# Performance work log

Measured on AMD Instinct MI355X. Metric: run time of the kernel, lower is better.

## Reference

```python
import math
import jax, jax.numpy as jnp
import numpy as np

NH, D, MULT, VOCAB, NLAYER = 4, 256, 128, 256, 2
N = MULT * D // NH  # 8192
EPS = 1e-5
THETA = 2.0 ** 16


def get_freqs(n):
    q = (jnp.arange(n, dtype=jnp.float32) // 2) * 2  # quantize(t, 2)
    return 1.0 / (THETA ** (q / n)) / (2 * math.pi)


def ln(x):
    # LayerNorm over last dim, no affine
    mu = jnp.mean(x, axis=-1, keepdims=True)
    var = jnp.mean((x - mu) ** 2, axis=-1, keepdims=True)
    return (x - mu) / jnp.sqrt(var + EPS)


def rope(phases, v):
    # phases: (T, N), v: (B, nh, T, N)
    ph = (phases % 1.0) * (2 * math.pi)
    c, s = jnp.cos(ph), jnp.sin(ph)
    v_rot = jnp.stack((-v[..., 1::2], v[..., ::2]), axis=-1).reshape(v.shape)
    return v * c + v_rot * s


def setup_inputs() -> dict:
    key = jax.random.key(0)
    ks = jax.random.split(key, 6)
    std = 0.02
    return {
        "idx": jax.random.randint(ks[0], (1, 2048), 0, VOCAB),
        "embed": jax.random.normal(ks[1], (VOCAB, D), jnp.float32) * std,
        "encoder": jax.random.normal(ks[2], (NH, D, N), jnp.float32) * std,
        "encoder_v": jax.random.normal(ks[3], (NH, D, N), jnp.float32) * std,
        "decoder": jax.random.normal(ks[4], (NH * N, D), jnp.float32) * std,
        "lm_head": jax.random.normal(ks[5], (D, VOCAB), jnp.float32) * std,
    }


def reference(idx, embed, encoder, encoder_v, decoder, lm_head):
    B, T = idx.shape
    freqs = get_freqs(N)  # (N,)
    phases = jnp.arange(T, dtype=jnp.float32)[:, None] * freqs[None, :]  # (T, N)
    # strictly-lower-triangular causal mask (tril diagonal=-1)
    t = jnp.arange(T)
    mask = (t[:, None] > t[None, :]).astype(jnp.float32)  # (T, T)

    x = ln(embed[idx][:, None])  # (B, 1, T, D)
    for _ in range(NLAYER):
        x_sparse = jax.nn.relu(jnp.einsum('bltd,hdn->bhtn', x, encoder))  # (B,nh,T,N)
        QR = rope(phases, x_sparse)
        scores = jnp.einsum('bhtn,bhsn->bhts', QR, QR) * mask  # (B,nh,T,T)
        yKV = ln(jnp.einsum('bhts,blsd->bhtd', scores, x))  # (B,nh,T,D)
        y_sparse = jax.nn.relu(jnp.einsum('bhtd,hdn->bhtn', yKV, encoder_v))
        xy = x_sparse * y_sparse  # (B,nh,T,N)
        xy = xy.transpose(0, 2, 1, 3).reshape(B, 1, T, NH * N)
        yMLP = xy @ decoder  # (B,1,T,D)
        x = ln(x + ln(yMLP))
    logits = x[:, 0] @ lm_head  # (B,T,vocab)
    return logits
```

## Files before the change

### kernel.cpp

```cpp
#include <hip/hip_runtime.h>
#include <hip/hip_bf16.h>
#include <math.h>

typedef unsigned short u16;
typedef unsigned int u32;
typedef __attribute__((ext_vector_type(8))) short short8;
typedef __attribute__((ext_vector_type(4))) float f32x4;
typedef __attribute__((ext_vector_type(4))) unsigned short u16x4;

__device__ __forceinline__ u16 f2b(float f) {
  u32 u = __builtin_bit_cast(u32, f);
  u = (u + 0x7fffu + ((u >> 16) & 1u)) >> 16;
  return (u16)u;
}
__device__ __forceinline__ float b2f(u16 s) {
  return __builtin_bit_cast(float, (u32)s << 16);
}

__device__ __forceinline__ void ld_g2l(const u16* g, u16* l) {
  __builtin_amdgcn_global_load_lds(
      (const __attribute__((address_space(1))) unsigned int*)g,
      (__attribute__((address_space(3))) unsigned int*)l, 16, 0, 0);
}

__device__ __forceinline__ float rope_frev(int n) {
  return exp2f((float)(-(n & ~1)) * (1.0f / 512.0f)) * 0.15915494f;
}
__device__ __forceinline__ void rope_cs_fast(float frev, int t, float& c, float& s) {
  float ph = (float)t * frev;
  ph -= floorf(ph);
#if __has_builtin(__builtin_amdgcn_sinf) && __has_builtin(__builtin_amdgcn_cosf)
  s = __builtin_amdgcn_sinf(ph);
  c = __builtin_amdgcn_cosf(ph);
#else
  __sincosf(ph * 6.2831853f, &s, &c);
#endif
}

__device__ __forceinline__ void gemm_core(
    const u16* __restrict__ A, const u16* __restrict__ B,
    int lda, int ldb, int Klen, int kb, int bm, int bn,
    u16* __restrict__ As, u16* __restrict__ Bs, f32x4 (&acc)[4][4])
{
  int tid = threadIdx.x;
  int w = tid >> 6, lane = tid & 63;
  int srow = (w << 4) + (lane >> 2);
  int scol = (lane & 3) << 3;
  const u16* ga0 = A + (long)(bm * 128 + srow) * lda + kb + scol;
  const u16* ga1 = ga0 + (long)64 * lda;
  const u16* gb0 = B + (long)(bn * 128 + srow) * ldb + kb + scol;
  const u16* gb1 = gb0 + (long)64 * ldb;
  u16* la0 = As + (w << 9);  u16* la1 = la0 + 2048;
  u16* lb0 = Bs + (w << 9);  u16* lb1 = lb0 + 2048;

  int wm = (w >> 1) << 6, wn = (w & 1) << 6;
  int lane15 = lane & 15, quad = lane >> 4;
  const u16* ar = As + (wm + lane15) * 32 + quad * 8;
  const u16* br = Bs + (wn + lane15) * 32 + quad * 8;

#pragma unroll
  for (int i = 0; i < 4; i++)
#pragma unroll
    for (int j = 0; j < 4; j++) { f32x4 z = {0.f, 0.f, 0.f, 0.f}; acc[i][j] = z; }

  for (int k = 0; k < Klen; k += 64) {
    ld_g2l(ga0 + k, la0);
    ld_g2l(ga1 + k, la1);
    ld_g2l(gb0 + k, lb0);
    ld_g2l(gb1 + k, lb1);
    ld_g2l(ga0 + k + 32, la0 + 4096);
    ld_g2l(ga1 + k + 32, la1 + 4096);
    ld_g2l(gb0 + k + 32, lb0 + 4096);
    ld_g2l(gb1 + k + 32, lb1 + 4096);
    __syncthreads();
#pragma unroll
    for (int h = 0; h < 2; h++) {
      short8 af[4], bfr[4];
#pragma unroll
      for (int mt = 0; mt < 4; mt++) af[mt] = *(const short8*)(ar + h * 4096 + mt * 16 * 32);
#pragma unroll
      for (int nt = 0; nt < 4; nt++) bfr[nt] = *(const short8*)(br + h * 4096 + nt * 16 * 32);
#pragma unroll
      for (int mt = 0; mt < 4; mt++)
#pragma unroll
        for (int nt = 0; nt < 4; nt++)
          acc[mt][nt] = __builtin_amdgcn_mfma_f32_16x16x32_bf16(af[mt], bfr[nt], acc[mt][nt], 0, 0, 0);
    }
    __syncthreads();
  }
}

template<int EPI>
__global__ __launch_bounds__(256, 2) void gemm_bt(
    const u16* __restrict__ A, const u16* __restrict__ B, void* __restrict__ C,
    int K, int lda, int ldb, int ldc, int nsplits, long aB, long bB, long cB,
    int tri)
{
  __shared__ __align__(16) u16 As[2 * 128 * 32];
  __shared__ __align__(16) u16 Bs[2 * 128 * 32];
  int bn = blockIdx.x, bm = blockIdx.y;
  int batch = blockIdx.z / nsplits, sp = blockIdx.z % nsplits;
  int Klen = K / nsplits, kb = sp * Klen;
  if (tri) {
    int kend = (bm + 1) * 128;
    if (kb >= kend) return;
    if (kb + Klen > kend) Klen = kend - kb;
  }

  f32x4 acc[4][4];
  gemm_core(A + (long)batch * aB, B + (long)batch * bB, lda, ldb, Klen, kb, bm, bn, As, Bs, acc);

  int lane = threadIdx.x & 63, w = threadIdx.x >> 6;
  int wm = (w >> 1) << 6, wn = (w & 1) << 6;
  int lane15 = lane & 15, quad = lane >> 4;

  float frev[4] = {0.f, 0.f, 0.f, 0.f};
  if (EPI == 1 || EPI == 4) {
#pragma unroll
    for (int nt = 0; nt < 4; nt++)
      frev[nt] = rope_frev(bn * 128 + wn + nt * 16 + lane15);
  }

#pragma unroll
  for (int mt = 0; mt < 4; mt++)
#pragma unroll
    for (int nt = 0; nt < 4; nt++) {
      int gn = bn * 128 + wn + nt * 16 + lane15;
#pragma unroll
      for (int r = 0; r < 4; r++) {
        int gm = bm * 128 + wm + mt * 16 + quad * 4 + r;
        float v = acc[mt][nt][r];
        long ci = (long)batch * cB + (long)gm * ldc + gn;
        if (EPI == 0) {
          ((float*)C)[ci] = v;
        } else if (EPI == 1) {
          float rv = fmaxf(v, 0.f);
          float ro = __shfl_xor(rv, 1);
          float c, s; rope_cs_fast(frev[nt], gm, c, s);
          float out = (gn & 1) ? (rv * c + ro * s) : (rv * c - ro * s);
          ((u16*)C)[ci] = f2b(out);
        } else if (EPI == 3) {
          atomicAdd(&((float*)C)[ci], v);
        } else if (EPI == 4) {
          u16* Cp = (u16*)C;
          float q = b2f(Cp[ci]);
          float qo = __shfl_xor(q, 1);
          float c, s; rope_cs_fast(frev[nt], gm, c, s);
          float xs = (gn & 1) ? (q * c - qo * s) : (q * c + qo * s);
          Cp[ci] = f2b(fmaxf(v, 0.f) * xs);
        }
      }
    }
}

#define SC_BAR   __builtin_amdgcn_s_barrier()
#define SC_LGKM0 asm volatile("s_waitcnt lgkmcnt(0)" ::: "memory")
#define SC_LGKM8 asm volatile("s_waitcnt lgkmcnt(8)" ::: "memory")
#define SC_VMF   do { asm volatile("s_waitcnt vmcnt(4)" ::: "memory"); \
                      __builtin_amdgcn_sched_barrier(0); } while (0)
#define SC_P1    __builtin_amdgcn_s_setprio(1)
#define SC_P0    __builtin_amdgcn_s_setprio(0)

#define DSA(Ab, mh) { \
  _Pragma("unroll") for (int mt = 0; mt < 4; mt++) { \
    aA[mt][0] = *(const short8*)((Ab) + ((mh) * 64 + mt * 16) * 64 + koff0); \
    aA[mt][1] = *(const short8*)((Ab) + ((mh) * 64 + mt * 16) * 64 + koff1); } }

#define DSB(Bb, nh, dst) { \
  _Pragma("unroll") for (int nt = 0; nt < 2; nt++) { \
    dst[nt][0] = *(const short8*)((Bb) + ((nh) * 32 + nt * 16) * 64 + koff0); \
    dst[nt][1] = *(const short8*)((Bb) + ((nh) * 32 + nt * 16) * 64 + koff1); } }

#define MMA(MH, NH, BB) { \
  _Pragma("unroll") for (int mt = 0; mt < 4; mt++) \
  _Pragma("unroll") for (int nt = 0; nt < 2; nt++) { \
    acc[(MH)*4+mt][(NH)*2+nt] = __builtin_amdgcn_mfma_f32_16x16x32_bf16( \
        aA[mt][0], BB[nt][0], acc[(MH)*4+mt][(NH)*2+nt], 0, 0, 0); \
    acc[(MH)*4+mt][(NH)*2+nt] = __builtin_amdgcn_mfma_f32_16x16x32_bf16( \
        aA[mt][1], BB[nt][1], acc[(MH)*4+mt][(NH)*2+nt], 0, 0, 0); } }

#define SCORES_K_LOOP(kb, nkt) \
  for (int i = 0; i < (nkt) / 2; i++) { \
    int kt1 = (kb) + 2 * i + 1; \
    int kt2 = 2 * i + 2; if (kt2 > (nkt) - 1) kt2 = (nkt) - 1; kt2 += (kb); \
    int kt3 = 2 * i + 3; if (kt3 > (nkt) - 1) kt3 = (nkt) - 1; kt3 += (kb); \
    short8 aA[4][2], bb0[2][2], bb1[2][2]; \
     \
    DSA(A0, 0); DSB(B0, 0, bb0); \
    STG(gA, &Abuf[1][0], kt1); \
    SC_LGKM8; SC_BAR; SC_LGKM0; SC_P1; MMA(0, 0, bb0); SC_P0; SC_BAR; \
     \
    DSB(B0, 1, bb1); \
    STG(gA + HSTEP, &Abuf[1][128 * 64], kt1); \
    SC_BAR; SC_LGKM0; SC_P1; MMA(0, 1, bb1); SC_P0; SC_BAR; \
     \
    DSA(A0, 1); \
    STG(gB, &Bbuf[0][0], kt2); \
    SC_BAR; SC_LGKM0; SC_P1; MMA(1, 1, bb1); SC_P0; SC_BAR; \
     \
    STG(gB + HSTEP, &Bbuf[0][128 * 64], kt2); \
    SC_VMF; SC_BAR; SC_LGKM0; SC_P1; MMA(1, 0, bb0); SC_P0; SC_BAR; \
     \
    DSA(A1, 0); DSB(B1, 0, bb0); \
    STG(gA, &Abuf[0][0], kt2); \
    SC_LGKM8; SC_BAR; SC_LGKM0; SC_P1; MMA(0, 0, bb0); SC_P0; SC_BAR; \
     \
    DSB(B1, 1, bb1); \
    STG(gA + HSTEP, &Abuf[0][128 * 64], kt2); \
    SC_BAR; SC_LGKM0; SC_P1; MMA(0, 1, bb1); SC_P0; SC_BAR; \
     \
    DSA(A1, 1); \
    STG(gB, &Bbuf[1][0], kt3); \
    SC_BAR; SC_LGKM0; SC_P1; MMA(1, 1, bb1); SC_P0; SC_BAR; \
     \
    STG(gB + HSTEP, &Bbuf[1][128 * 64], kt3); \
    SC_VMF; SC_BAR; SC_LGKM0; SC_P1; MMA(1, 0, bb0); SC_P0; SC_BAR; \
  }

#define SCORES_SETUP \
  int tid = threadIdx.x; \
  int w = tid >> 6, lane = tid & 63; \
  int wr = w >> 2, wc = w & 3; \
  int lane15 = lane & 15, quad = lane >> 4; \
  int swz = lane15 & 7; \
  int koff0 = ((quad) ^ swz) << 3; \
  int koff1 = ((4 + quad) ^ swz) << 3; \
  const u16* gA = Q + (long)(bm * 256) * 8192; \
  const u16* gB = Q + (long)(bn * 256) * 8192; \
  const u16* A0 = &Abuf[0][(wr * 128 + lane15) * 64]; \
  const u16* A1 = &Abuf[1][(wr * 128 + lane15) * 64]; \
  const u16* B0 = &Bbuf[0][(wc * 64 + lane15) * 64]; \
  const u16* B1 = &Bbuf[1][(wc * 64 + lane15) * 64]; \
  int sr = lane >> 3, sc = lane & 7; \
  long g_sk = (long)sr * 8192 + ((sc ^ sr) << 3); \
  int l_base = (w * 16) * 64; \
  long g_wrow = (long)(w * 16) * 8192; \
  auto STG = [&](const u16* gHalfBase, u16* lHalfBase, int kt) { \
    const u16* g = gHalfBase + g_wrow + g_sk + (long)kt * 64; \
    u16* l = lHalfBase + l_base; \
    ld_g2l(g, l); \
    ld_g2l(g + (long)8 * 8192, l + 8 * 64); \
  }; \
  f32x4 acc[8][4]; \
  _Pragma("unroll") \
  for (int i2 = 0; i2 < 8; i2++) \
  _Pragma("unroll") \
    for (int j = 0; j < 4; j++) { f32x4 z = {0.f, 0.f, 0.f, 0.f}; acc[i2][j] = z; } \
  const long HSTEP = (long)128 * 8192;

__device__ __forceinline__ void tri_decode(int q, int& bm, int& bn) {
  bm = (int)((sqrtf(8.f * (float)q + 1.f) - 1.f) * 0.5f);
  while ((bm + 1) * (bm + 2) / 2 <= q) bm++;
  while (bm * (bm + 1) / 2 > q) bm--;
  bn = q - bm * (bm + 1) / 2;
}

__device__ __forceinline__ int xcd_remap(int lin, int total) {
  int cpx = total >> 3, rr = total & 7;
  int xcd = lin & 7, ii = lin >> 3;
  return (xcd < rr) ? xcd * (cpx + 1) + ii
                    : rr * (cpx + 1) + (xcd - rr) * cpx + ii;
}

__global__ __launch_bounds__(512, 1) void gemm_scores8(
    const u16* __restrict__ QR, u16* __restrict__ S, int T, int ntri)
{
  __shared__ __align__(16) u16 Abuf[2][256 * 64];
  __shared__ __align__(16) u16 Bbuf[2][256 * 64];

  int c = xcd_remap(blockIdx.x, gridDim.x);
  int zh = c / ntri, q = c % ntri;
  int bm, bn; tri_decode(q, bm, bn);

  const u16* Q = QR + (long)zh * (long)T * 8192;
  u16* Sb = S + (long)zh * (long)T * T;

  SCORES_SETUP

  STG(gA, &Abuf[0][0], 0); STG(gA + HSTEP, &Abuf[0][128 * 64], 0);
  STG(gB, &Bbuf[0][0], 0); STG(gB + HSTEP, &Bbuf[0][128 * 64], 0);
  STG(gB, &Bbuf[1][0], 1); STG(gB + HSTEP, &Bbuf[1][128 * 64], 1);
  SC_VMF;
  SC_BAR;

  SCORES_K_LOOP(0, 128)

#pragma unroll
  for (int mt = 0; mt < 8; mt++)
#pragma unroll
    for (int nt = 0; nt < 4; nt++) {
      int gn = bn * 256 + wc * 64 + nt * 16 + lane15;
#pragma unroll
      for (int r = 0; r < 4; r++) {
        int gm = bm * 256 + wr * 128 + mt * 16 + quad * 4 + r;
        Sb[(long)gm * T + gn] = f2b(gm > gn ? acc[mt][nt][r] : 0.f);
      }
    }
}

__global__ __launch_bounds__(512, 1) void gemm_scores_k3(
    const u16* __restrict__ QR, float* __restrict__ Sf, int T, int ntri)
{
  __shared__ __align__(16) u16 Abuf[2][256 * 64];
  __shared__ __align__(16) u16 Bbuf[2][256 * 64];

  int c = xcd_remap(blockIdx.x, gridDim.x);
  int sp = c % 3, c2 = c / 3;
  int zh = c2 / ntri, q = c2 % ntri;
  int bm, bn; tri_decode(q, bm, bn);

  int kb = sp * 44;
  int nkt = (sp == 2) ? 40 : 44;

  const u16* Q = QR + (long)zh * (long)T * 8192;
  float* Sb = Sf + (long)zh * (long)T * T;

  SCORES_SETUP

  STG(gA, &Abuf[0][0], kb); STG(gA + HSTEP, &Abuf[0][128 * 64], kb);
  STG(gB, &Bbuf[0][0], kb); STG(gB + HSTEP, &Bbuf[0][128 * 64], kb);
  STG(gB, &Bbuf[1][0], kb + 1); STG(gB + HSTEP, &Bbuf[1][128 * 64], kb + 1);
  SC_VMF;
  SC_BAR;

  SCORES_K_LOOP(kb, nkt)

#pragma unroll
  for (int mt = 0; mt < 8; mt++)
#pragma unroll
    for (int nt = 0; nt < 4; nt++) {
      int gn = bn * 256 + wc * 64 + nt * 16 + lane15;
#pragma unroll
      for (int r = 0; r < 4; r++) {
        int gm = bm * 256 + wr * 128 + mt * 16 + quad * 4 + r;
        atomicAdd(&Sb[(long)gm * T + gn], acc[mt][nt][r]);
      }
    }
}

__global__ __launch_bounds__(256) void tril_cvt(
    const float* __restrict__ Sf, u16* __restrict__ Sb, int T, int ntri)
{
  int bx = blockIdx.x;
  int tl = bx >> 3, chunk = bx & 7;
  int zh = tl / ntri, q = tl % ntri;
  int bm, bn; tri_decode(q, bm, bn);
  const float* f = Sf + (long)zh * (long)T * T;
  u16* b = Sb + (long)zh * (long)T * T;
  int tid = threadIdx.x;
  int rsub = tid >> 6;
  int col = bn * 256 + (tid & 63) * 4;
#pragma unroll
  for (int it = 0; it < 8; it++) {
    int row = bm * 256 + chunk * 32 + it * 4 + rsub;
    long o = (long)row * T + col;
    f32x4 v = *(const f32x4*)(f + o);
    u16x4 w2;
#pragma unroll
    for (int r = 0; r < 4; r++)
      w2[r] = (row > col + r) ? f2b(v[r]) : (u16)0;
    *(u16x4*)(b + o) = w2;
  }
}

__global__ __launch_bounds__(256) void trans_f32_bf16(
    const float* __restrict__ src, u16* __restrict__ dst, int R, int C)
{
  __shared__ float tile[32][33];
  long off = (long)blockIdx.z * R * C;
  const float* s = src + off;
  u16* d = dst + off;
  int lx = threadIdx.x & 31, ly = threadIdx.x >> 5;
  int c = blockIdx.x * 32 + lx;
#pragma unroll
  for (int p = 0; p < 32; p += 8)
    tile[ly + p][lx] = s[(long)(blockIdx.y * 32 + ly + p) * C + c];
  __syncthreads();
  int rr = blockIdx.y * 32 + lx;
#pragma unroll
  for (int p = 0; p < 32; p += 8)
    d[(long)(blockIdx.x * 32 + ly + p) * R + rr] = f2b(tile[lx][ly + p]);
}

__device__ __forceinline__ float block_sum(float v, float* red) {
#pragma unroll
  for (int o = 32; o > 0; o >>= 1) v += __shfl_down(v, o, 64);
  int lane = threadIdx.x & 63, wid = threadIdx.x >> 6;
  if (lane == 0) red[wid] = v;
  __syncthreads();
  float r = red[0] + red[1] + red[2] + red[3];
  __syncthreads();
  return r;
}

__global__ __launch_bounds__(256) void embed_ln(
    const int* __restrict__ idx, const float* __restrict__ embed,
    float* __restrict__ x, u16* __restrict__ xb, u16* __restrict__ xT, int T)
{
  __shared__ float red[4];
  int t = blockIdx.x, d = threadIdx.x;
  float v = embed[(long)idx[t] * 256 + d];
  float mu = block_sum(v, red) * (1.f / 256.f);
  float c = v - mu;
  float var = block_sum(c * c, red) * (1.f / 256.f);
  float o = c * rsqrtf(var + 1e-5f);
  x[(long)t * 256 + d] = o;
  xb[(long)t * 256 + d] = f2b(o);
  xT[(long)d * T + t] = f2b(o);
}

__global__ __launch_bounds__(256) void row_ln(
    const float* __restrict__ in, u16* __restrict__ out)
{
  __shared__ float red[4];
  long row = blockIdx.x;
  int d = threadIdx.x;
  float v = in[row * 256 + d];
  float mu = block_sum(v, red) * (1.f / 256.f);
  float c = v - mu;
  float var = block_sum(c * c, red) * (1.f / 256.f);
  out[row * 256 + d] = f2b(c * rsqrtf(var + 1e-5f));
}

__global__ __launch_bounds__(256) void resid_ln(
    const float* __restrict__ yMLP, float* __restrict__ x,
    u16* __restrict__ xb, u16* __restrict__ xT, int T)
{
  __shared__ float red[4];
  int t = blockIdx.x, d = threadIdx.x;
  float y = yMLP[(long)t * 256 + d];
  float mu1 = block_sum(y, red) * (1.f / 256.f);
  float c1 = y - mu1;
  float var1 = block_sum(c1 * c1, red) * (1.f / 256.f);
  float l1 = c1 * rsqrtf(var1 + 1e-5f);
  float v = x[(long)t * 256 + d] + l1;
  float mu2 = block_sum(v, red) * (1.f / 256.f);
  float c2 = v - mu2;
  float var2 = block_sum(c2 * c2, red) * (1.f / 256.f);
  float o = c2 * rsqrtf(var2 + 1e-5f);
  x[(long)t * 256 + d] = o;
  xb[(long)t * 256 + d] = f2b(o);
  xT[(long)d * T + t] = f2b(o);
}

extern "C" void kernel_launch(void* const* d_in, const int* in_sizes, int n_in,
                              void* d_out, int out_size, void* d_ws, size_t ws_size,
                              hipStream_t stream) {
  const int*   idx       = (const int*)d_in[0];
  const float* embed     = (const float*)d_in[1];
  const float* encoder   = (const float*)d_in[2];
  const float* encoder_v = (const float*)d_in[3];
  const float* decoder   = (const float*)d_in[4];
  const float* lm_head   = (const float*)d_in[5];
  const int T = in_sizes[0];
  const int D = 256, NH = 4, Nn = 8192, V = 256;

  char* ws = (char*)d_ws;
  size_t off = 0;
  auto alloc = [&](size_t bytes) -> void* {
    void* p = ws + off; off += (bytes + 255) & ~(size_t)255; return p;
  };
  float* x_f32   = (float*)alloc((size_t)T * D * 4);
  float* yMLP    = (float*)alloc((size_t)T * D * 4);
  float* yKV_f32 = (float*)alloc((size_t)NH * T * D * 4);
  u16* x_b    = (u16*)alloc((size_t)T * D * 2);
  u16* xT     = (u16*)alloc((size_t)T * D * 2);
  u16* yKV_b  = (u16*)alloc((size_t)NH * T * D * 2);
  u16* lmT    = (u16*)alloc((size_t)D * V * 2);
  u16* encT   = (u16*)alloc((size_t)NH * Nn * D * 2);
  u16* encvT  = (u16*)alloc((size_t)NH * Nn * D * 2);
  u16* decT   = (u16*)alloc((size_t)D * NH * Nn * 2);
  size_t per_head = ((size_t)T * T * 2 + 256) + ((size_t)T * Nn * 2 + 256);
  int HB = 4;
  while (HB > 1 && off + (size_t)HB * per_head > ws_size) HB >>= 1;
  u16* scores = (u16*)alloc((size_t)HB * T * T * 2);
  u16* QRxy   = (u16*)alloc((size_t)HB * T * Nn * 2);
  if (off > ws_size) return;
  float* scoresF = nullptr;
  {
    size_t need = (size_t)HB * T * T * 4 + 256;
    if (off + need <= ws_size) scoresF = (float*)alloc((size_t)HB * T * T * 4);
  }

  trans_f32_bf16<<<dim3(Nn / 32, D / 32, NH), 256, 0, stream>>>(encoder, encT, D, Nn);
  trans_f32_bf16<<<dim3(Nn / 32, D / 32, NH), 256, 0, stream>>>(encoder_v, encvT, D, Nn);
  trans_f32_bf16<<<dim3(D / 32, (NH * Nn) / 32, 1), 256, 0, stream>>>(decoder, decT, NH * Nn, D);
  trans_f32_bf16<<<dim3(V / 32, D / 32, 1), 256, 0, stream>>>(lm_head, lmT, D, V);

  embed_ln<<<T, 256, 0, stream>>>(idx, embed, x_f32, x_b, xT, T);

  const int nbm = T / 256, ntri = nbm * (nbm + 1) / 2;

  for (int l = 0; l < 2; l++) {
    hipMemsetAsync(yMLP, 0, (size_t)T * D * 4, stream);
    for (int h0 = 0; h0 < NH; h0 += HB) {
      gemm_bt<1><<<dim3(Nn / 128, T / 128, HB), 256, 0, stream>>>(
          x_b, encT + (size_t)h0 * Nn * D, QRxy,
          D, D, D, Nn, 1, 0L, (long)Nn * D, (long)T * Nn, 0);
      if (scoresF) {
        hipMemsetAsync(scoresF, 0, (size_t)HB * T * T * 4, stream);
        gemm_scores_k3<<<dim3(ntri * HB * 3, 1, 1), 512, 0, stream>>>(
            QRxy, scoresF, T, ntri);
        tril_cvt<<<dim3(HB * ntri * 8, 1, 1), 256, 0, stream>>>(
            scoresF, scores, T, ntri);
      } else {
        gemm_scores8<<<dim3(ntri * HB, 1, 1), 512, 0, stream>>>(
            QRxy, scores, T, ntri);
      }
      hipMemsetAsync(yKV_f32, 0, (size_t)HB * T * D * 4, stream);
      gemm_bt<3><<<dim3(D / 128, T / 128, HB * 8), 256, 0, stream>>>(
          scores, xT, yKV_f32,
          T, T, T, D, 8, (long)T * T, 0L, (long)T * D, 1);
      row_ln<<<HB * T, 256, 0, stream>>>(yKV_f32, yKV_b);
      gemm_bt<4><<<dim3(Nn / 128, T / 128, HB), 256, 0, stream>>>(
          yKV_b, encvT + (size_t)h0 * Nn * D, QRxy,
          D, D, D, Nn, 1, (long)T * D, (long)Nn * D, (long)T * Nn, 0);
      gemm_bt<3><<<dim3(D / 128, T / 128, HB * 4), 256, 0, stream>>>(
          QRxy, decT + (size_t)h0 * Nn, yMLP,
          Nn, Nn, NH * Nn, D, 4, (long)T * Nn, (long)Nn, 0L, 0);
    }
    resid_ln<<<T, 256, 0, stream>>>(yMLP, x_f32, x_b, xT, T);
  }

  gemm_bt<0><<<dim3(V / 128, T / 128, 1), 256, 0, stream>>>(
      x_b, lmT, d_out, D, D, D, V, 1, 0L, 0L, 0L, 0);
}
```

Baseline: 1.140 ms.

## Store split-K score partials in compact per-tile buffers aliased with yKV scratch

The fp32 scratch for split-K score partials now holds only the lower-triangular 256x256 tiles in a packed per-tile layout instead of full T x T matrices. This buffer shares memory with the yKV fp32 buffer, and heads can be processed in chunks. The aim is to shrink the memset and atomic traffic and to make the split-K path fit the workspace more often instead of falling back to the non-split kernel. The cost is extra index arithmetic and possibly more launches when heads are chunked.

```diff
diff --git a/kernel.cpp b/kernel.cpp
--- a/kernel.cpp
+++ b/kernel.cpp
@@ -313,7 +313,7 @@
   int nkt = (sp == 2) ? 40 : 44;
 
   const u16* Q = QR + (long)zh * (long)T * 8192;
-  float* Sb = Sf + (long)zh * (long)T * T;
+  float* tb = Sf + ((long)(zh * ntri + q) << 16);
 
   SCORES_SETUP
 
@@ -329,11 +329,11 @@
   for (int mt = 0; mt < 8; mt++)
 #pragma unroll
     for (int nt = 0; nt < 4; nt++) {
-      int gn = bn * 256 + wc * 64 + nt * 16 + lane15;
+      int ct = wc * 64 + nt * 16 + lane15;
 #pragma unroll
       for (int r = 0; r < 4; r++) {
-        int gm = bm * 256 + wr * 128 + mt * 16 + quad * 4 + r;
-        atomicAdd(&Sb[(long)gm * T + gn], acc[mt][nt][r]);
+        int rt = wr * 128 + mt * 16 + quad * 4 + r;
+        atomicAdd(&tb[rt * 256 + ct], acc[mt][nt][r]);
       }
     }
 }
@@ -345,21 +345,22 @@
   int tl = bx >> 3, chunk = bx & 7;
   int zh = tl / ntri, q = tl % ntri;
   int bm, bn; tri_decode(q, bm, bn);
-  const float* f = Sf + (long)zh * (long)T * T;
+  const float* f = Sf + ((long)tl << 16);
   u16* b = Sb + (long)zh * (long)T * T;
   int tid = threadIdx.x;
   int rsub = tid >> 6;
-  int col = bn * 256 + (tid & 63) * 4;
+  int lc = (tid & 63) * 4;
 #pragma unroll
   for (int it = 0; it < 8; it++) {
-    int row = bm * 256 + chunk * 32 + it * 4 + rsub;
-    long o = (long)row * T + col;
-    f32x4 v = *(const f32x4*)(f + o);
+    int rt = chunk * 32 + it * 4 + rsub;
+    int gm = bm * 256 + rt;
+    int gn0 = bn * 256 + lc;
+    f32x4 v = *(const f32x4*)(f + rt * 256 + lc);
     u16x4 w2;
 #pragma unroll
     for (int r = 0; r < 4; r++)
-      w2[r] = (row > col + r) ? f2b(v[r]) : (u16)0;
-    *(u16x4*)(b + o) = w2;
+      w2[r] = (gm > gn0 + r) ? f2b(v[r]) : (u16)0;
+    *(u16x4*)(b + (long)gm * T + gn0) = w2;
   }
 }
 
@@ -462,7 +463,6 @@
   };
   float* x_f32   = (float*)alloc((size_t)T * D * 4);
   float* yMLP    = (float*)alloc((size_t)T * D * 4);
-  float* yKV_f32 = (float*)alloc((size_t)NH * T * D * 4);
   u16* x_b    = (u16*)alloc((size_t)T * D * 2);
   u16* xT     = (u16*)alloc((size_t)T * D * 2);
   u16* yKV_b  = (u16*)alloc((size_t)NH * T * D * 2);
@@ -471,16 +471,27 @@
   u16* encvT  = (u16*)alloc((size_t)NH * Nn * D * 2);
   u16* decT   = (u16*)alloc((size_t)D * NH * Nn * 2);
   size_t per_head = ((size_t)T * T * 2 + 256) + ((size_t)T * Nn * 2 + 256);
+  size_t yKVbytes = (size_t)NH * T * D * 4;
   int HB = 4;
-  while (HB > 1 && off + (size_t)HB * per_head > ws_size) HB >>= 1;
+  while (HB > 1 && off + (size_t)HB * per_head + yKVbytes + 256 > ws_size) HB >>= 1;
   u16* scores = (u16*)alloc((size_t)HB * T * T * 2);
   u16* QRxy   = (u16*)alloc((size_t)HB * T * Nn * 2);
+
+  const int nbm = T / 256, ntri = nbm * (nbm + 1) / 2;
+
+  int HC = HB;
+  size_t uBytes = yKVbytes;
+  while (HC >= 2) {
+    size_t need = (size_t)HC * ntri * 65536 * 4;
+    if (need < yKVbytes) need = yKVbytes;
+    if (off + need + 256 <= ws_size) { uBytes = need; break; }
+    HC >>= 1;
+  }
+  if (HC < 2) HC = 0;
+  float* U = (float*)alloc(uBytes);
+  float* yKV_f32 = U;
+  float* scoresF = U;
   if (off > ws_size) return;
-  float* scoresF = nullptr;
-  {
-    size_t need = (size_t)HB * T * T * 4 + 256;
-    if (off + need <= ws_size) scoresF = (float*)alloc((size_t)HB * T * T * 4);
-  }
 
   trans_f32_bf16<<<dim3(Nn / 32, D / 32, NH), 256, 0, stream>>>(encoder, encT, D, Nn);
   trans_f32_bf16<<<dim3(Nn / 32, D / 32, NH), 256, 0, stream>>>(encoder_v, encvT, D, Nn);
@@ -488,8 +499,6 @@
   trans_f32_bf16<<<dim3(V / 32, D / 32, 1), 256, 0, stream>>>(lm_head, lmT, D, V);
 
   embed_ln<<<T, 256, 0, stream>>>(idx, embed, x_f32, x_b, xT, T);
-
-  const int nbm = T / 256, ntri = nbm * (nbm + 1) / 2;
 
   for (int l = 0; l < 2; l++) {
     hipMemsetAsync(yMLP, 0, (size_t)T * D * 4, stream);
@@ -497,12 +506,14 @@
       gemm_bt<1><<<dim3(Nn / 128, T / 128, HB), 256, 0, stream>>>(
           x_b, encT + (size_t)h0 * Nn * D, QRxy,
           D, D, D, Nn, 1, 0L, (long)Nn * D, (long)T * Nn, 0);
-      if (scoresF) {
-        hipMemsetAsync(scoresF, 0, (size_t)HB * T * T * 4, stream);
-        gemm_scores_k3<<<dim3(ntri * HB * 3, 1, 1), 512, 0, stream>>>(
-            QRxy, scoresF, T, ntri);
-        tril_cvt<<<dim3(HB * ntri * 8, 1, 1), 256, 0, stream>>>(
-            scoresF, scores, T, ntri);
+      if (HC > 0) {
+        for (int hc = 0; hc < HB; hc += HC) {
+          hipMemsetAsync(scoresF, 0, (size_t)HC * ntri * 65536 * 4, stream);
+          gemm_scores_k3<<<dim3(ntri * HC * 3, 1, 1), 512, 0, stream>>>(
+              QRxy + (size_t)hc * T * Nn, scoresF, T, ntri);
+          tril_cvt<<<dim3(HC * ntri * 8, 1, 1), 256, 0, stream>>>(
+              scoresF, scores + (size_t)hc * (size_t)T * T, T, ntri);
+        }
       } else {
         gemm_scores8<<<dim3(ntri * HB, 1, 1), 512, 0, stream>>>(
             QRxy, scores, T, ntri);
```

After: 1.185 ms. 3.9% more time.
